# Optimization experiments

Measured on AMD Instinct MI355X. Metric: run time of the kernel, lower is better.

Reference implementation:

```python
import jax, jax.numpy as jnp
import numpy as np

B, S, H, V, E = 64, 20, 128, 50257, 300


def gru(p, x, h):
    # tf.contrib.rnn.GRUCell: r,u = sigmoid([x,h]@Wg + bg); c = tanh([x, r*h]@Wc + bc); h' = u*h + (1-u)*c
    gk, gb, ck, cb = p
    xh = jnp.concatenate([x, h], axis=-1)
    r, u = jnp.split(jax.nn.sigmoid(xh @ gk + gb), 2, axis=-1)
    c = jnp.tanh(jnp.concatenate([x, r * h], axis=-1) @ ck + cb)
    return u * h + (1.0 - u) * c


def setup_inputs() -> dict:
    key = jax.random.key(0)
    ks = jax.random.split(key, 32)
    s = 0.08
    rn = lambda k, shp: (jax.random.normal(k, shp, jnp.float32) * s)
    inp = {}
    inp['x'] = jax.random.randint(ks[0], (B, S), 0, V, dtype=jnp.int32)
    inp['x_length'] = jax.random.randint(ks[1], (B,), 1, S + 1, dtype=jnp.int32)
    inp['y'] = jax.random.randint(ks[2], (B, S), 0, V, dtype=jnp.int32)
    inp['y_length'] = jax.random.randint(ks[3], (B,), 1, S + 1, dtype=jnp.int32)
    inp['embedding'] = jax.random.normal(ks[4], (V, E), jnp.float32) * 0.1
    # encoder GRU: layer0 in=E, layer1 in=H
    inp['e0_gk'] = rn(ks[5], (E + H, 2 * H)); inp['e0_gb'] = rn(ks[6], (2 * H,))
    inp['e0_ck'] = rn(ks[7], (E + H, H));     inp['e0_cb'] = rn(ks[8], (H,))
    inp['e1_gk'] = rn(ks[9], (2 * H, 2 * H)); inp['e1_gb'] = rn(ks[10], (2 * H,))
    inp['e1_ck'] = rn(ks[11], (2 * H, H));    inp['e1_cb'] = rn(ks[12], (H,))
    # decoder GRU: layer0 in = E + attention_size(H) = E+H, layer1 in=H
    inp['d0_gk'] = rn(ks[13], (E + 2 * H, 2 * H)); inp['d0_gb'] = rn(ks[14], (2 * H,))
    inp['d0_ck'] = rn(ks[15], (E + 2 * H, H));     inp['d0_cb'] = rn(ks[16], (H,))
    inp['d1_gk'] = rn(ks[17], (2 * H, 2 * H));     inp['d1_gb'] = rn(ks[18], (2 * H,))
    inp['d1_ck'] = rn(ks[19], (2 * H, H));         inp['d1_cb'] = rn(ks[20], (H,))
    # Bahdanau attention (num_units=H) + attention output layer + vocab projection
    inp['W_mem'] = rn(ks[21], (H, H))
    inp['W_q'] = rn(ks[22], (H, H))
    inp['v_att'] = rn(ks[23], (H,))
    inp['W_attn'] = rn(ks[24], (2 * H, H))
    inp['W_proj'] = rn(ks[25], (H, V))
    inp['b_proj'] = jnp.zeros((V,), jnp.float32)
    return inp


def _forward(x, x_length, y, y_length, embedding,
             e0_gk, e0_gb, e0_ck, e0_cb, e1_gk, e1_gb, e1_ck, e1_cb,
             d0_gk, d0_gb, d0_ck, d0_cb, d1_gk, d1_gb, d1_ck, d1_cb,
             W_mem, W_q, v_att, W_attn, W_proj, b_proj):
    e0 = (e0_gk, e0_gb, e0_ck, e0_cb)
    e1 = (e1_gk, e1_gb, e1_ck, e1_cb)
    d0 = (d0_gk, d0_gb, d0_ck, d0_cb)
    d1 = (d1_gk, d1_gb, d1_ck, d1_cb)
    t_idx = jnp.arange(S)
    x_valid = t_idx[None, :] < x_length[:, None]   # [B,S]
    y_valid = t_idx[None, :] < y_length[:, None]   # [B,S]

    # ---- encoder: 2-layer GRU dynamic_rnn with sequence_length semantics ----
    ex = embedding[x]                               # [B,S,E]
    zeros = jnp.zeros((x.shape[0], H), embedding.dtype)

    def enc_step(carry, inp_t):
        h0, h1 = carry
        xt, vt = inp_t                              # xt [B,E], vt [B,1]
        n0 = gru(e0, xt, h0)
        n1 = gru(e1, n0, h1)
        n0 = jnp.where(vt, n0, h0)                  # copy-through past seq end
        n1 = jnp.where(vt, n1, h1)
        return (n0, n1), jnp.where(vt, n1, 0.0)     # outputs zeroed past seq end

    (h0f, h1f), mem = jax.lax.scan(
        enc_step, (zeros, zeros),
        (ex.transpose(1, 0, 2), x_valid.T[:, :, None]))
    memory = mem.transpose(1, 0, 2)                 # [B,S,H] encoder outputs

    # ---- Bahdanau attention precompute ----
    keys = jnp.einsum('bsh,hu->bsu', memory, W_mem)  # memory_layer(memory)
    neg_inf = jnp.finfo(memory.dtype).min

    # ---- attention decoder (TrainingHelper) ----
    ey = embedding[y]                               # [B,S,E]
    attn0 = jnp.zeros((x.shape[0], H), embedding.dtype)

    def dec_step(carry, inp_t):
        h0, h1, attn = carry
        yt, vt = inp_t                              # yt [B,E], vt [B,1]
        ci = jnp.concatenate([yt, attn], axis=-1)   # cell input = [emb, prev attention]
        n0 = gru(d0, ci, h0)
        n1 = gru(d1, n0, h1)
        q = n1 @ W_q                                # query_layer(cell_output)
        sc = jnp.einsum('bsu,u->bs', jnp.tanh(keys + q[:, None, :]), v_att)
        sc = jnp.where(x_valid, sc, neg_inf)        # memory_sequence_length mask
        al = jax.nn.softmax(sc, axis=-1)            # [B,S]
        ctx = jnp.einsum('bs,bsh->bh', al, memory)  # context
        na = jnp.concatenate([n1, ctx], axis=-1) @ W_attn  # attention_layer (no bias)
        logits = na @ W_proj + b_proj               # projection_layer
        logits = jnp.where(vt, logits, 0.0)         # dynamic_decode zeroes finished emits
        return (n0, n1, na), logits

    _, logits = jax.lax.scan(
        dec_step, (h0f, h1f, attn0),
        (ey.transpose(1, 0, 2), y_valid.T[:, :, None]))
    return logits.transpose(1, 0, 2)                # [B,S,V] rnn_output


def reference(x, x_length, y, y_length, embedding,
              e0_gk, e0_gb, e0_ck, e0_cb, e1_gk, e1_gb, e1_ck, e1_cb,
              d0_gk, d0_gb, d0_ck, d0_cb, d1_gk, d1_gb, d1_ck, d1_cb,
              W_mem, W_q, v_att, W_attn, W_proj, b_proj):
    return _forward(x, x_length, y, y_length, embedding,
                    e0_gk, e0_gb, e0_ck, e0_cb, e1_gk, e1_gb, e1_ck, e1_cb,
                    d0_gk, d0_gb, d0_ck, d0_cb, d1_gk, d1_gb, d1_ck, d1_cb,
                    W_mem, W_q, v_att, W_attn, W_proj, b_proj)
```

## Files before the change

### kernel.cpp

```cpp
#include <hip/hip_runtime.h>
#include <hip/hip_bf16.h>

#define Bb 64
#define Ss 20
#define Hh 128
#define Vv 50257
#define Ee 300
#define Vpad 50304

typedef short bf16x8 __attribute__((ext_vector_type(8)));
typedef float f32x4 __attribute__((ext_vector_type(4)));

__device__ __forceinline__ unsigned short f2bf(float f){
  unsigned u = __float_as_uint(f);
  u += 0x7fff + ((u >> 16) & 1);
  return (unsigned short)(u >> 16);
}
__device__ __forceinline__ float sigm(float x){ return 1.f / (1.f + __expf(-x)); }
__device__ __forceinline__ float tanh_fast(float x){
  float e = __expf(2.f * x);
  return 1.f - 2.f / (e + 1.f);
}

template<int K4>
__device__ __forceinline__ float dotT(const float* __restrict__ w, const float* v){
  float a0 = 0.f, a1 = 0.f, a2 = 0.f, a3 = 0.f;
  const float4* w4 = (const float4*)w;
  const float4* v4 = (const float4*)v;
#pragma unroll
  for (int i = 0; i < K4; i++){
    float4 wv = w4[i]; float4 xv = v4[i];
    a0 = fmaf(wv.x, xv.x, a0); a1 = fmaf(wv.y, xv.y, a1);
    a2 = fmaf(wv.z, xv.z, a2); a3 = fmaf(wv.w, xv.w, a3);
  }
  return (a0 + a1) + (a2 + a3);
}


struct TMat { const float* src; float* dst; int r0, R, C; };
struct TList { TMat m[15]; };

__global__ __launch_bounds__(256) void wtrans_kernel(TList L){
  TMat t = L.m[blockIdx.y];
  int idx = blockIdx.x * 256 + threadIdx.x;
  int total = t.R * t.C;
  if (idx >= total) return;
  int o = idx / t.R;
  int i = idx - o * t.R;
  t.dst[idx] = t.src[(size_t)(t.r0 + i) * t.C + o];
}

__global__ __launch_bounds__(256) void wpt_kernel(const float* __restrict__ Wp,
                                                  unsigned short* __restrict__ Wpt){
  __shared__ unsigned short tile[64][136];
  int n0 = blockIdx.x * 64;
  int tid = threadIdx.x;
  for (int idx = tid; idx < 8192; idx += 256){
    int k = idx >> 6, nn = idx & 63;
    int n = n0 + nn;
    float f = (n < Vv) ? Wp[(size_t)k * Vv + n] : 0.f;
    tile[nn][k] = f2bf(f);
  }
  __syncthreads();
  for (int idx = tid; idx < 1024; idx += 256){
    int nn = idx >> 4, c = idx & 15;
    uint4 v = *reinterpret_cast<const uint4*>(&tile[nn][c * 8]);
    *reinterpret_cast<uint4*>(Wpt + (((size_t)(n0 + nn)) << 7) + c * 8) = v;
  }
}


__global__ __launch_bounds__(256) void pre_kernel(
    const int* __restrict__ x, const int* __restrict__ y, const float* __restrict__ emb,
    const float* __restrict__ egx, const float* __restrict__ ecx,
    const float* __restrict__ egb, const float* __restrict__ ecb,
    const float* __restrict__ dgx, const float* __restrict__ dcx,
    const float* __restrict__ dgb, const float* __restrict__ dcb,
    float* __restrict__ epg, float* __restrict__ epc,
    float* __restrict__ dpg, float* __restrict__ dpc)
{
  __shared__ __align__(16) float er[Ee];
  int tid = threadIdx.x, ti = blockIdx.x, which = blockIdx.y;
  int tok = which ? y[ti] : x[ti];
  if (tid < 75)
    ((float4*)er)[tid] = ((const float4*)(emb + (size_t)tok * Ee))[tid];
  __syncthreads();
  const float* gx = which ? dgx : egx;
  const float* cx = which ? dcx : ecx;
  float accg = (which ? dgb : egb)[tid] + dotT<75>(gx + (size_t)tid * Ee, er);
  (which ? dpg : epg)[ti * 256 + tid] = accg;
  if (tid < 128){
    float accc = (which ? dcb : ecb)[tid] + dotT<75>(cx + (size_t)tid * Ee, er);
    (which ? dpc : epc)[ti * 128 + tid] = accc;
  }
}


__global__ __launch_bounds__(256, 1) void recur2(
    const int* __restrict__ xlen,
    const float* __restrict__ epg, const float* __restrict__ epc,
    const float* __restrict__ dpg, const float* __restrict__ dpc,
    const float* __restrict__ e0_gh_t, const float* __restrict__ e0_ch_t,
    const float* __restrict__ e1_g_t, const float* __restrict__ e1_c_t,
    const float* __restrict__ e1_gb,  const float* __restrict__ e1_cb,
    const float* __restrict__ d0_gah_t, const float* __restrict__ d0_cah_t,
    const float* __restrict__ d1_g_t, const float* __restrict__ d1_c_t,
    const float* __restrict__ d1_gb,  const float* __restrict__ d1_cb,
    const float* __restrict__ W_mem_t, const float* __restrict__ W_q_t,
    const float* __restrict__ W_attn_t, const float* __restrict__ v_att,
    unsigned short* __restrict__ na_bf)
{
  __shared__ __align__(16) float mem_s[Ss][Hh];
  __shared__ __align__(16) float keys_s[Ss][132];
  __shared__ __align__(16) float h0[Hh], h1[Hh], attn[Hh], n0[Hh], n1[Hh], rh[Hh], q[Hh], ctx[Hh];
  __shared__ __align__(16) float gates[2*Hh];
  __shared__ __align__(16) float vatt_s[Hh];
  __shared__ float part[Ss][8], als[Ss];

  const int tid = threadIdx.x, b = blockIdx.x;
  if (tid < Hh){ h0[tid] = 0.f; h1[tid] = 0.f; attn[tid] = 0.f; vatt_s[tid] = v_att[tid]; }
  __syncthreads();
  const int xl = xlen[b];

  for (int t = 0; t < Ss; t++){
    const int tix = b * Ss + t;
    float g = epg[(tix << 8) + tid] + dotT<32>(e0_gh_t + tid * 128, h0);
    gates[tid] = sigm(g);
    __syncthreads();
    if (tid < Hh) rh[tid] = gates[tid] * h0[tid];
    __syncthreads();
    {
      int o = tid >> 1, half = tid & 1;
      float a = dotT<16>(e0_ch_t + o * 128 + half * 64, rh + half * 64);
      a += __shfl_xor(a, 1);
      if (!half){
        float c = tanh_fast(epc[(tix << 7) + o] + a);
        float u = gates[128 + o];
        n0[o] = u * h0[o] + (1.f - u) * c;
      }
    }
    __syncthreads();
    float g1 = e1_gb[tid] + dotT<32>(e1_g_t + tid * 256, n0)
                          + dotT<32>(e1_g_t + tid * 256 + 128, h1);
    gates[tid] = sigm(g1);
    __syncthreads();
    if (tid < Hh) rh[tid] = gates[tid] * h1[tid];
    __syncthreads();
    {
      int o = tid >> 1, half = tid & 1;
      const float* base = e1_c_t + o * 256 + half * 128;
      float a = half ? dotT<32>(base, rh) : dotT<32>(base, n0);
      a += __shfl_xor(a, 1);
      if (!half){
        float c = tanh_fast(e1_cb[o] + a);
        float u = gates[128 + o];
        float nh = u * h1[o] + (1.f - u) * c;
        bool v = (t < xl);
        mem_s[t][o] = v ? nh : 0.f;
        h1[o] = v ? nh : h1[o];
        h0[o] = v ? n0[o] : h0[o];
      }
    }
    __syncthreads();
  }

  for (int idx = tid; idx < Ss * Hh; idx += 256){
    int s = idx >> 7, j = idx & 127;
    keys_s[s][j] = dotT<32>(W_mem_t + j * 128, mem_s[s]);
  }
  __syncthreads();

  for (int t = 0; t < Ss; t++){
    const int tix = b * Ss + t;
    float g = dpg[(tix << 8) + tid] + dotT<32>(d0_gah_t + tid * 256, attn)
                                    + dotT<32>(d0_gah_t + tid * 256 + 128, h0);
    gates[tid] = sigm(g);
    __syncthreads();
    if (tid < Hh) rh[tid] = gates[tid] * h0[tid];
    __syncthreads();
    {
      int o = tid >> 1, half = tid & 1;
      const float* base = d0_cah_t + o * 256 + half * 128;
      float a = half ? dotT<32>(base, rh) : dotT<32>(base, attn);
      a += __shfl_xor(a, 1);
      if (!half){
        float c = tanh_fast(dpc[(tix << 7) + o] + a);
        float u = gates[128 + o];
        float nv = u * h0[o] + (1.f - u) * c;
        n0[o] = nv; h0[o] = nv;
      }
    }
    __syncthreads();
    float g1 = d1_gb[tid] + dotT<32>(d1_g_t + tid * 256, n0)
                          + dotT<32>(d1_g_t + tid * 256 + 128, h1);
    gates[tid] = sigm(g1);
    __syncthreads();
    if (tid < Hh) rh[tid] = gates[tid] * h1[tid];
    __syncthreads();
    {
      int o = tid >> 1, half = tid & 1;
      const float* base = d1_c_t + o * 256 + half * 128;
      float a = half ? dotT<32>(base, rh) : dotT<32>(base, n0);
      a += __shfl_xor(a, 1);
      if (!half){
        float c = tanh_fast(d1_cb[o] + a);
        float u = gates[128 + o];
        float nh = u * h1[o] + (1.f - u) * c;
        n1[o] = nh; h1[o] = nh;
      }
    }
    __syncthreads();
    {
      int o = tid >> 1, half = tid & 1;
      float a = dotT<16>(W_q_t + o * 128 + half * 64, n1 + half * 64);
      a += __shfl_xor(a, 1);
      if (!half) q[o] = a;
    }
    __syncthreads();
    if (tid < Ss * 8){
      int s = tid >> 3, p = tid & 7;
      float a = 0.f;
#pragma unroll
      for (int c2 = 0; c2 < 16; c2++){
        int u2 = p * 16 + c2;
        a += tanh_fast(keys_s[s][u2] + q[u2]) * vatt_s[u2];
      }
      part[s][p] = a;
    }
    __syncthreads();
    if (tid < 64){
      int s = tid;
      bool valid = (s < Ss) && (s < xl);
      float sc = -3.4e38f;
      if (valid){ sc = 0.f;
#pragma unroll
        for (int p = 0; p < 8; p++) sc += part[s][p];
      }
      float mx = sc;
#pragma unroll
      for (int off = 32; off >= 1; off >>= 1) mx = fmaxf(mx, __shfl_xor(mx, off));
      float e = valid ? __expf(sc - mx) : 0.f;
      float sm = e;
#pragma unroll
      for (int off = 32; off >= 1; off >>= 1) sm += __shfl_xor(sm, off);
      if (s < Ss) als[s] = e / sm;
    }
    __syncthreads();
    if (tid < Hh){
      float a = 0.f;
#pragma unroll
      for (int s = 0; s < Ss; s++) a += als[s] * mem_s[s][tid];
      ctx[tid] = a;
    }
    __syncthreads();
    {
      int o = tid >> 1, half = tid & 1;
      const float* base = W_attn_t + o * 256 + half * 128;
      float a = half ? dotT<32>(base, ctx) : dotT<32>(base, n1);
      a += __shfl_xor(a, 1);
      if (!half){
        attn[o] = a;
        na_bf[(tix << 7) + o] = f2bf(a);
      }
    }
    __syncthreads();
  }
}


__global__ __launch_bounds__(256) void proj2(
    const unsigned short* __restrict__ na_bf, const unsigned short* __restrict__ Wpt,
    const float* __restrict__ b_proj, const int* __restrict__ ylen,
    float* __restrict__ out)
{
  __shared__ int yl_s[Bb];
  const int tid = threadIdx.x;
  if (tid < Bb) yl_s[tid] = ylen[tid];
  const int n0 = blockIdx.x * 128, m0 = blockIdx.y * 64;
  const int lane = tid & 63, w = tid >> 6, lm = lane & 15, qq = lane >> 4;

  f32x4 acc[4][2];
#pragma unroll
  for (int mt = 0; mt < 4; mt++){ acc[mt][0] = (f32x4){0,0,0,0}; acc[mt][1] = (f32x4){0,0,0,0}; }

#pragma unroll
  for (int ks = 0; ks < 4; ks++){
    int ko = ks * 32 + qq * 8;
    bf16x8 b0 = *(const bf16x8*)(Wpt + (((size_t)(n0 + w*32 + lm)) << 7) + ko);
    bf16x8 b1 = *(const bf16x8*)(Wpt + (((size_t)(n0 + w*32 + 16 + lm)) << 7) + ko);
#pragma unroll
    for (int mt = 0; mt < 4; mt++){
      bf16x8 a = *(const bf16x8*)(na_bf + (((size_t)(m0 + mt*16 + lm)) << 7) + ko);
      acc[mt][0] = __builtin_amdgcn_mfma_f32_16x16x32_bf16(a, b0, acc[mt][0], 0, 0, 0);
      acc[mt][1] = __builtin_amdgcn_mfma_f32_16x16x32_bf16(a, b1, acc[mt][1], 0, 0, 0);
    }
  }
  __syncthreads();

#pragma unroll
  for (int mt = 0; mt < 4; mt++){
    int row = m0 + mt*16 + qq*4;
#pragma unroll
    for (int n2 = 0; n2 < 2; n2++){
      int col = n0 + w*32 + n2*16 + lm;
      if (col < Vv){
        float bp = b_proj[col];
#pragma unroll
        for (int r = 0; r < 4; r++){
          int rr = row + r;
          int bb = rr / Ss;
          int tt = rr - bb * Ss;
          float val = (tt < yl_s[bb]) ? (acc[mt][n2][r] + bp) : 0.f;
          out[(size_t)rr * Vv + col] = val;
        }
      }
    }
  }
}

extern "C" void kernel_launch(void* const* d_in, const int* in_sizes, int n_in,
                              void* d_out, int out_size, void* d_ws, size_t ws_size,
                              hipStream_t stream) {
  const int*   x        = (const int*)d_in[0];
  const int*   x_length = (const int*)d_in[1];
  const int*   y        = (const int*)d_in[2];
  const int*   y_length = (const int*)d_in[3];
  const float* emb      = (const float*)d_in[4];
  const float* e0_gk = (const float*)d_in[5];  const float* e0_gb = (const float*)d_in[6];
  const float* e0_ck = (const float*)d_in[7];  const float* e0_cb = (const float*)d_in[8];
  const float* e1_gk = (const float*)d_in[9];  const float* e1_gb = (const float*)d_in[10];
  const float* e1_ck = (const float*)d_in[11]; const float* e1_cb = (const float*)d_in[12];
  const float* d0_gk = (const float*)d_in[13]; const float* d0_gb = (const float*)d_in[14];
  const float* d0_ck = (const float*)d_in[15]; const float* d0_cb = (const float*)d_in[16];
  const float* d1_gk = (const float*)d_in[17]; const float* d1_gb = (const float*)d_in[18];
  const float* d1_ck = (const float*)d_in[19]; const float* d1_cb = (const float*)d_in[20];
  const float* W_mem = (const float*)d_in[21]; const float* W_q   = (const float*)d_in[22];
  const float* v_att = (const float*)d_in[23]; const float* W_attn= (const float*)d_in[24];
  const float* W_proj= (const float*)d_in[25]; const float* b_proj= (const float*)d_in[26];
  float* out = (float*)d_out;

  size_t off = 0;
  auto alloc = [&](size_t bytes) -> void* {
    void* p = (char*)d_ws + off;
    off += (bytes + 255) & ~(size_t)255;
    return p;
  };
  unsigned short* Wpt   = (unsigned short*)alloc((size_t)Vpad * 128 * 2);
  unsigned short* na_bf = (unsigned short*)alloc((size_t)Bb * Ss * Hh * 2);
  float* epg = (float*)alloc((size_t)Bb*Ss*256*4);
  float* epc = (float*)alloc((size_t)Bb*Ss*128*4);
  float* dpg = (float*)alloc((size_t)Bb*Ss*256*4);
  float* dpc = (float*)alloc((size_t)Bb*Ss*128*4);
  float* e0_gx_t  = (float*)alloc(256*300*4);
  float* e0_gh_t  = (float*)alloc(256*128*4);
  float* e0_cx_t  = (float*)alloc(128*300*4);
  float* e0_ch_t  = (float*)alloc(128*128*4);
  float* e1_g_t   = (float*)alloc(256*256*4);
  float* e1_c_t   = (float*)alloc(128*256*4);
  float* d0_gx_t  = (float*)alloc(256*300*4);
  float* d0_gah_t = (float*)alloc(256*256*4);
  float* d0_cx_t  = (float*)alloc(128*300*4);
  float* d0_cah_t = (float*)alloc(128*256*4);
  float* d1_g_t   = (float*)alloc(256*256*4);
  float* d1_c_t   = (float*)alloc(128*256*4);
  float* W_mem_t  = (float*)alloc(128*128*4);
  float* W_q_t    = (float*)alloc(128*128*4);
  float* W_attn_t = (float*)alloc(128*256*4);

  TList L;
  L.m[0]  = { e0_gk, e0_gx_t,    0, 300, 256 };
  L.m[1]  = { e0_gk, e0_gh_t,  300, 128, 256 };
  L.m[2]  = { e0_ck, e0_cx_t,    0, 300, 128 };
  L.m[3]  = { e0_ck, e0_ch_t,  300, 128, 128 };
  L.m[4]  = { e1_gk, e1_g_t,     0, 256, 256 };
  L.m[5]  = { e1_ck, e1_c_t,     0, 256, 128 };
  L.m[6]  = { d0_gk, d0_gx_t,    0, 300, 256 };
  L.m[7]  = { d0_gk, d0_gah_t, 300, 256, 256 };
  L.m[8]  = { d0_ck, d0_cx_t,    0, 300, 128 };
  L.m[9]  = { d0_ck, d0_cah_t, 300, 256, 128 };
  L.m[10] = { d1_gk, d1_g_t,     0, 256, 256 };
  L.m[11] = { d1_ck, d1_c_t,     0, 256, 128 };
  L.m[12] = { W_mem, W_mem_t,    0, 128, 128 };
  L.m[13] = { W_q,   W_q_t,      0, 128, 128 };
  L.m[14] = { W_attn,W_attn_t,   0, 256, 128 };

  wtrans_kernel<<<dim3(300, 15), 256, 0, stream>>>(L);
  wpt_kernel<<<Vpad / 64, 256, 0, stream>>>(W_proj, Wpt);
  pre_kernel<<<dim3(Bb * Ss, 2), 256, 0, stream>>>(
      x, y, emb, e0_gx_t, e0_cx_t, e0_gb, e0_cb,
      d0_gx_t, d0_cx_t, d0_gb, d0_cb, epg, epc, dpg, dpc);
  recur2<<<Bb, 256, 0, stream>>>(
      x_length, epg, epc, dpg, dpc,
      e0_gh_t, e0_ch_t, e1_g_t, e1_c_t, e1_gb, e1_cb,
      d0_gah_t, d0_cah_t, d1_g_t, d1_c_t, d1_gb, d1_cb,
      W_mem_t, W_q_t, W_attn_t, v_att, na_bf);
  proj2<<<dim3(Vpad / 128, (Bb * Ss) / 64), 256, 0, stream>>>(
      na_bf, Wpt, b_proj, y_length, out);
}
```

Measured before the change: 1.515 ms.

## Pack recurrent weights as interleaved bf16, restructure GRU steps, retile projection GEMM

```diff
diff --git a/kernel.cpp b/kernel.cpp
--- a/kernel.cpp
+++ b/kernel.cpp
@@ -16,45 +16,59 @@
   u += 0x7fff + ((u >> 16) & 1);
   return (unsigned short)(u >> 16);
 }
+__device__ __forceinline__ float blo(unsigned u){ return __uint_as_float(u << 16); }
+__device__ __forceinline__ float bhi(unsigned u){ return __uint_as_float(u & 0xffff0000u); }
 __device__ __forceinline__ float sigm(float x){ return 1.f / (1.f + __expf(-x)); }
 __device__ __forceinline__ float tanh_fast(float x){
   float e = __expf(2.f * x);
   return 1.f - 2.f / (e + 1.f);
 }
 
-template<int K4>
-__device__ __forceinline__ float dotT(const float* __restrict__ w, const float* v){
-  float a0 = 0.f, a1 = 0.f, a2 = 0.f, a3 = 0.f;
-  const float4* w4 = (const float4*)w;
-  const float4* v4 = (const float4*)v;
-#pragma unroll
-  for (int i = 0; i < K4; i++){
-    float4 wv = w4[i]; float4 xv = v4[i];
-    a0 = fmaf(wv.x, xv.x, a0); a1 = fmaf(wv.y, xv.y, a1);
-    a2 = fmaf(wv.z, xv.z, a2); a3 = fmaf(wv.w, xv.w, a3);
+template<int K8, int O>
+__device__ __forceinline__ float dotP(const uint4* __restrict__ wp, int o, const float* x){
+  float a0=0.f, a1=0.f, a2=0.f, a3=0.f;
+  const float4* x4 = (const float4*)x;
+#pragma unroll
+  for (int kk = 0; kk < K8; kk++){
+    uint4 u = wp[kk*O + o];
+    float4 xa = x4[2*kk], xb = x4[2*kk+1];
+    a0 = fmaf(blo(u.x), xa.x, a0); a1 = fmaf(bhi(u.x), xa.y, a1);
+    a2 = fmaf(blo(u.y), xa.z, a2); a3 = fmaf(bhi(u.y), xa.w, a3);
+    a0 = fmaf(blo(u.z), xb.x, a0); a1 = fmaf(bhi(u.z), xb.y, a1);
+    a2 = fmaf(blo(u.w), xb.z, a2); a3 = fmaf(bhi(u.w), xb.w, a3);
   }
   return (a0 + a1) + (a2 + a3);
 }
 
 
-struct TMat { const float* src; float* dst; int r0, R, C; };
-struct TList { TMat m[15]; };
-
-__global__ __launch_bounds__(256) void wtrans_kernel(TList L){
-  TMat t = L.m[blockIdx.y];
+struct PD { const float* src; uint4* dst; int r0, K, O; };
+struct PL { PD m[15]; };
+
+__global__ __launch_bounds__(256) void pack_kernel(PL L){
+  PD p = L.m[blockIdx.y];
+  int K8 = (p.K + 7) >> 3;
   int idx = blockIdx.x * 256 + threadIdx.x;
-  int total = t.R * t.C;
-  if (idx >= total) return;
-  int o = idx / t.R;
-  int i = idx - o * t.R;
-  t.dst[idx] = t.src[(size_t)(t.r0 + i) * t.C + o];
-}
-
-__global__ __launch_bounds__(256) void wpt_kernel(const float* __restrict__ Wp,
-                                                  unsigned short* __restrict__ Wpt){
+  if (idx >= K8 * p.O) return;
+  int kk = idx / p.O, o = idx - kk * p.O;
+  unsigned w[8];
+#pragma unroll
+  for (int j = 0; j < 8; j++){
+    int k = 8*kk + j;
+    float f = (k < p.K) ? p.src[(size_t)(p.r0 + k) * p.O + o] : 0.f;
+    w[j] = f2bf(f);
+  }
+  uint4 u;
+  u.x = w[0] | (w[1] << 16);
+  u.y = w[2] | (w[3] << 16);
+  u.z = w[4] | (w[5] << 16);
+  u.w = w[6] | (w[7] << 16);
+  p.dst[idx] = u;
+}
+
+__global__ __launch_bounds__(256) void wpt2_kernel(const float* __restrict__ Wp,
+                                                   unsigned short* __restrict__ W2){
   __shared__ unsigned short tile[64][136];
-  int n0 = blockIdx.x * 64;
-  int tid = threadIdx.x;
+  int n0 = blockIdx.x * 64, tid = threadIdx.x;
   for (int idx = tid; idx < 8192; idx += 256){
     int k = idx >> 6, nn = idx & 63;
     int n = n0 + nn;
@@ -63,159 +77,140 @@
   }
   __syncthreads();
   for (int idx = tid; idx < 1024; idx += 256){
-    int nn = idx >> 4, c = idx & 15;
+    int c = idx >> 6, nn = idx & 63;
     uint4 v = *reinterpret_cast<const uint4*>(&tile[nn][c * 8]);
-    *reinterpret_cast<uint4*>(Wpt + (((size_t)(n0 + nn)) << 7) + c * 8) = v;
-  }
-}
-
-
-__global__ __launch_bounds__(256) void pre_kernel(
+    int n = n0 + nn;
+    size_t dst = (((size_t)(n >> 4) * 16 + c) * 16 + (n & 15)) * 8;
+    *reinterpret_cast<uint4*>(W2 + dst) = v;
+  }
+}
+
+
+__global__ __launch_bounds__(256) void pre2(
     const int* __restrict__ x, const int* __restrict__ y, const float* __restrict__ emb,
-    const float* __restrict__ egx, const float* __restrict__ ecx,
+    const uint4* __restrict__ egx, const uint4* __restrict__ ecx,
     const float* __restrict__ egb, const float* __restrict__ ecb,
-    const float* __restrict__ dgx, const float* __restrict__ dcx,
+    const uint4* __restrict__ dgx, const uint4* __restrict__ dcx,
     const float* __restrict__ dgb, const float* __restrict__ dcb,
     float* __restrict__ epg, float* __restrict__ epc,
     float* __restrict__ dpg, float* __restrict__ dpc)
 {
-  __shared__ __align__(16) float er[Ee];
+  __shared__ __align__(16) float er[304];
   int tid = threadIdx.x, ti = blockIdx.x, which = blockIdx.y;
   int tok = which ? y[ti] : x[ti];
   if (tid < 75)
     ((float4*)er)[tid] = ((const float4*)(emb + (size_t)tok * Ee))[tid];
+  if (tid < 4) er[300 + tid] = 0.f;
   __syncthreads();
-  const float* gx = which ? dgx : egx;
-  const float* cx = which ? dcx : ecx;
-  float accg = (which ? dgb : egb)[tid] + dotT<75>(gx + (size_t)tid * Ee, er);
-  (which ? dpg : epg)[ti * 256 + tid] = accg;
+  const uint4* gx = which ? dgx : egx;
+  const uint4* cx = which ? dcx : ecx;
+  float g = (which ? dgb : egb)[tid] + dotP<38,256>(gx, tid, er);
+  (which ? dpg : epg)[ti * 256 + tid] = g;
   if (tid < 128){
-    float accc = (which ? dcb : ecb)[tid] + dotT<75>(cx + (size_t)tid * Ee, er);
-    (which ? dpc : epc)[ti * 128 + tid] = accc;
-  }
-}
-
-
-__global__ __launch_bounds__(256, 1) void recur2(
+    float c = (which ? dcb : ecb)[tid] + dotP<38,128>(cx, tid, er);
+    (which ? dpc : epc)[ti * 128 + tid] = c;
+  }
+}
+
+
+__global__ __launch_bounds__(256, 1) void recur3(
     const int* __restrict__ xlen,
     const float* __restrict__ epg, const float* __restrict__ epc,
     const float* __restrict__ dpg, const float* __restrict__ dpc,
-    const float* __restrict__ e0_gh_t, const float* __restrict__ e0_ch_t,
-    const float* __restrict__ e1_g_t, const float* __restrict__ e1_c_t,
-    const float* __restrict__ e1_gb,  const float* __restrict__ e1_cb,
-    const float* __restrict__ d0_gah_t, const float* __restrict__ d0_cah_t,
-    const float* __restrict__ d1_g_t, const float* __restrict__ d1_c_t,
-    const float* __restrict__ d1_gb,  const float* __restrict__ d1_cb,
-    const float* __restrict__ W_mem_t, const float* __restrict__ W_q_t,
-    const float* __restrict__ W_attn_t, const float* __restrict__ v_att,
-    unsigned short* __restrict__ na_bf)
+    const uint4* __restrict__ e0g, const uint4* __restrict__ e0c,
+    const uint4* __restrict__ e1g, const uint4* __restrict__ e1c,
+    const float* __restrict__ e1_gb, const float* __restrict__ e1_cb,
+    const uint4* __restrict__ d0g, const uint4* __restrict__ d0c,
+    const uint4* __restrict__ d1g, const uint4* __restrict__ d1c,
+    const float* __restrict__ d1_gb, const float* __restrict__ d1_cb,
+    const uint4* __restrict__ wm, const uint4* __restrict__ wq,
+    const uint4* __restrict__ wat, const float* __restrict__ v_att,
+    unsigned short* __restrict__ na2)
 {
   __shared__ __align__(16) float mem_s[Ss][Hh];
   __shared__ __align__(16) float keys_s[Ss][132];
-  __shared__ __align__(16) float h0[Hh], h1[Hh], attn[Hh], n0[Hh], n1[Hh], rh[Hh], q[Hh], ctx[Hh];
-  __shared__ __align__(16) float gates[2*Hh];
+  __shared__ __align__(16) float h0[Hh];
+  __shared__ __align__(16) float cat0[256], cat0c[256], cat1[256], cat1c[256], catA[256];
+  __shared__ __align__(16) float gates[256];
+  __shared__ __align__(16) float qv[Hh];
   __shared__ __align__(16) float vatt_s[Hh];
   __shared__ float part[Ss][8], als[Ss];
 
   const int tid = threadIdx.x, b = blockIdx.x;
-  if (tid < Hh){ h0[tid] = 0.f; h1[tid] = 0.f; attn[tid] = 0.f; vatt_s[tid] = v_att[tid]; }
+  if (tid < 128){ h0[tid] = 0.f; cat1[128 + tid] = 0.f; vatt_s[tid] = v_att[tid]; }
   __syncthreads();
   const int xl = xlen[b];
 
   for (int t = 0; t < Ss; t++){
     const int tix = b * Ss + t;
-    float g = epg[(tix << 8) + tid] + dotT<32>(e0_gh_t + tid * 128, h0);
-    gates[tid] = sigm(g);
-    __syncthreads();
-    if (tid < Hh) rh[tid] = gates[tid] * h0[tid];
-    __syncthreads();
     {
-      int o = tid >> 1, half = tid & 1;
-      float a = dotT<16>(e0_ch_t + o * 128 + half * 64, rh + half * 64);
-      a += __shfl_xor(a, 1);
-      if (!half){
-        float c = tanh_fast(epc[(tix << 7) + o] + a);
-        float u = gates[128 + o];
-        n0[o] = u * h0[o] + (1.f - u) * c;
-      }
-    }
-    __syncthreads();
-    float g1 = e1_gb[tid] + dotT<32>(e1_g_t + tid * 256, n0)
-                          + dotT<32>(e1_g_t + tid * 256 + 128, h1);
-    gates[tid] = sigm(g1);
-    __syncthreads();
-    if (tid < Hh) rh[tid] = gates[tid] * h1[tid];
+      float gs = sigm(epg[tix * 256 + tid] + dotP<16,256>(e0g, tid, h0));
+      gates[tid] = gs;
+      if (tid < 128) cat0c[tid] = gs * h0[tid];
+    }
+    __syncthreads();
+    if (tid < 128){
+      float c = tanh_fast(epc[tix * 128 + tid] + dotP<16,128>(e0c, tid, cat0c));
+      float u = gates[128 + tid];
+      cat1[tid] = u * h0[tid] + (1.f - u) * c;
+    }
     __syncthreads();
     {
-      int o = tid >> 1, half = tid & 1;
-      const float* base = e1_c_t + o * 256 + half * 128;
-      float a = half ? dotT<32>(base, rh) : dotT<32>(base, n0);
-      a += __shfl_xor(a, 1);
-      if (!half){
-        float c = tanh_fast(e1_cb[o] + a);
-        float u = gates[128 + o];
-        float nh = u * h1[o] + (1.f - u) * c;
-        bool v = (t < xl);
-        mem_s[t][o] = v ? nh : 0.f;
-        h1[o] = v ? nh : h1[o];
-        h0[o] = v ? n0[o] : h0[o];
-      }
+      float gs = sigm(e1_gb[tid] + dotP<32,256>(e1g, tid, cat1));
+      gates[tid] = gs;
+      if (tid < 128){ cat1c[tid] = cat1[tid]; cat1c[128 + tid] = gs * cat1[128 + tid]; }
+    }
+    __syncthreads();
+    if (tid < 128){
+      float c = tanh_fast(e1_cb[tid] + dotP<32,128>(e1c, tid, cat1c));
+      float u = gates[128 + tid];
+      float h1o = cat1[128 + tid];
+      float nh = u * h1o + (1.f - u) * c;
+      bool v = (t < xl);
+      mem_s[t][tid] = v ? nh : 0.f;
+      cat1[128 + tid] = v ? nh : h1o;
+      h0[tid] = v ? cat1[tid] : h0[tid];
     }
     __syncthreads();
   }
 
   for (int idx = tid; idx < Ss * Hh; idx += 256){
     int s = idx >> 7, j = idx & 127;
-    keys_s[s][j] = dotT<32>(W_mem_t + j * 128, mem_s[s]);
-  }
+    keys_s[s][j] = dotP<16,128>(wm, j, mem_s[s]);
+  }
+  if (tid < 128){ cat0[tid] = 0.f; cat0[128 + tid] = h0[tid]; }
   __syncthreads();
 
   for (int t = 0; t < Ss; t++){
     const int tix = b * Ss + t;
-    float g = dpg[(tix << 8) + tid] + dotT<32>(d0_gah_t + tid * 256, attn)
-                                    + dotT<32>(d0_gah_t + tid * 256 + 128, h0);
-    gates[tid] = sigm(g);
-    __syncthreads();
-    if (tid < Hh) rh[tid] = gates[tid] * h0[tid];
-    __syncthreads();
     {
-      int o = tid >> 1, half = tid & 1;
-      const float* base = d0_cah_t + o * 256 + half * 128;
-      float a = half ? dotT<32>(base, rh) : dotT<32>(base, attn);
-      a += __shfl_xor(a, 1);
-      if (!half){
-        float c = tanh_fast(dpc[(tix << 7) + o] + a);
-        float u = gates[128 + o];
-        float nv = u * h0[o] + (1.f - u) * c;
-        n0[o] = nv; h0[o] = nv;
-      }
-    }
-    __syncthreads();
-    float g1 = d1_gb[tid] + dotT<32>(d1_g_t + tid * 256, n0)
-                          + dotT<32>(d1_g_t + tid * 256 + 128, h1);
-    gates[tid] = sigm(g1);
-    __syncthreads();
-    if (tid < Hh) rh[tid] = gates[tid] * h1[tid];
+      float gs = sigm(dpg[tix * 256 + tid] + dotP<32,256>(d0g, tid, cat0));
+      gates[tid] = gs;
+      if (tid < 128){ cat0c[tid] = cat0[tid]; cat0c[128 + tid] = gs * cat0[128 + tid]; }
+    }
+    __syncthreads();
+    if (tid < 128){
+      float c = tanh_fast(dpc[tix * 128 + tid] + dotP<32,128>(d0c, tid, cat0c));
+      float u = gates[128 + tid];
+      float nv = u * cat0[128 + tid] + (1.f - u) * c;
+      cat1[tid] = nv; cat0[128 + tid] = nv;
+    }
     __syncthreads();
     {
-      int o = tid >> 1, half = tid & 1;
-      const float* base = d1_c_t + o * 256 + half * 128;
-      float a = half ? dotT<32>(base, rh) : dotT<32>(base, n0);
-      a += __shfl_xor(a, 1);
-      if (!half){
-        float c = tanh_fast(d1_cb[o] + a);
-        float u = gates[128 + o];
-        float nh = u * h1[o] + (1.f - u) * c;
-        n1[o] = nh; h1[o] = nh;
-      }
-    }
-    __syncthreads();
-    {
-      int o = tid >> 1, half = tid & 1;
-      float a = dotT<16>(W_q_t + o * 128 + half * 64, n1 + half * 64);
-      a += __shfl_xor(a, 1);
-      if (!half) q[o] = a;
-    }
+      float gs = sigm(d1_gb[tid] + dotP<32,256>(d1g, tid, cat1));
+      gates[tid] = gs;
+      if (tid < 128){ cat1c[tid] = cat1[tid]; cat1c[128 + tid] = gs * cat1[128 + tid]; }
+    }
+    __syncthreads();
+    if (tid < 128){
+      float c = tanh_fast(d1_cb[tid] + dotP<32,128>(d1c, tid, cat1c));
+      float u = gates[128 + tid];
+      float h1o = cat1[128 + tid];
+      float nh = u * h1o + (1.f - u) * c;
+      catA[tid] = nh; cat1[128 + tid] = nh;
+    }
+    __syncthreads();
+    if (tid < 128) qv[tid] = dotP<16,128>(wq, tid, catA);
     __syncthreads();
     if (tid < Ss * 8){
       int s = tid >> 3, p = tid & 7;
@@ -223,7 +218,7 @@
 #pragma unroll
       for (int c2 = 0; c2 < 16; c2++){
         int u2 = p * 16 + c2;
-        a += tanh_fast(keys_s[s][u2] + q[u2]) * vatt_s[u2];
+        a += tanh_fast(keys_s[s][u2] + qv[u2]) * vatt_s[u2];
       }
       part[s][p] = a;
     }
@@ -246,73 +241,80 @@
       if (s < Ss) als[s] = e / sm;
     }
     __syncthreads();
-    if (tid < Hh){
+    if (tid < 128){
       float a = 0.f;
 #pragma unroll
       for (int s = 0; s < Ss; s++) a += als[s] * mem_s[s][tid];
-      ctx[tid] = a;
-    }
-    __syncthreads();
-    {
-      int o = tid >> 1, half = tid & 1;
-      const float* base = W_attn_t + o * 256 + half * 128;
-      float a = half ? dotT<32>(base, ctx) : dotT<32>(base, n1);
-      a += __shfl_xor(a, 1);
-      if (!half){
-        attn[o] = a;
-        na_bf[(tix << 7) + o] = f2bf(a);
-      }
-    }
-    __syncthreads();
-  }
-}
-
-
-__global__ __launch_bounds__(256) void proj2(
-    const unsigned short* __restrict__ na_bf, const unsigned short* __restrict__ Wpt,
+      catA[128 + tid] = a;
+    }
+    __syncthreads();
+    if (tid < 128){
+      float a = dotP<32,128>(wat, tid, catA);
+      cat0[tid] = a;
+      na2[(((size_t)(tix >> 4) * 16 + (tid >> 3)) * 16 + (tix & 15)) * 8 + (tid & 7)] = f2bf(a);
+    }
+    __syncthreads();
+  }
+}
+
+
+__global__ __launch_bounds__(256) void proj3(
+    const unsigned short* __restrict__ A2, const unsigned short* __restrict__ W2,
     const float* __restrict__ b_proj, const int* __restrict__ ylen,
     float* __restrict__ out)
 {
   __shared__ int yl_s[Bb];
   const int tid = threadIdx.x;
   if (tid < Bb) yl_s[tid] = ylen[tid];
-  const int n0 = blockIdx.x * 128, m0 = blockIdx.y * 64;
-  const int lane = tid & 63, w = tid >> 6, lm = lane & 15, qq = lane >> 4;
-
-  f32x4 acc[4][2];
-#pragma unroll
-  for (int mt = 0; mt < 4; mt++){ acc[mt][0] = (f32x4){0,0,0,0}; acc[mt][1] = (f32x4){0,0,0,0}; }
+  __syncthreads();
+  const int n0 = blockIdx.x * 128, m0 = blockIdx.y * 128;
+  const int w = tid >> 6, lane = tid & 63, lm = lane & 15, qq = lane >> 4;
+  const int wr = w >> 1, wc = w & 1;
+  const int mtb = (m0 >> 4) + wr * 4, ntb = (n0 >> 4) + wc * 4;
+
+  f32x4 acc[4][4];
+#pragma unroll
+  for (int mt = 0; mt < 4; mt++)
+#pragma unroll
+    for (int nt = 0; nt < 4; nt++) acc[mt][nt] = (f32x4){0.f,0.f,0.f,0.f};
 
 #pragma unroll
   for (int ks = 0; ks < 4; ks++){
-    int ko = ks * 32 + qq * 8;
-    bf16x8 b0 = *(const bf16x8*)(Wpt + (((size_t)(n0 + w*32 + lm)) << 7) + ko);
-    bf16x8 b1 = *(const bf16x8*)(Wpt + (((size_t)(n0 + w*32 + 16 + lm)) << 7) + ko);
-#pragma unroll
-    for (int mt = 0; mt < 4; mt++){
-      bf16x8 a = *(const bf16x8*)(na_bf + (((size_t)(m0 + mt*16 + lm)) << 7) + ko);
-      acc[mt][0] = __builtin_amdgcn_mfma_f32_16x16x32_bf16(a, b0, acc[mt][0], 0, 0, 0);
-      acc[mt][1] = __builtin_amdgcn_mfma_f32_16x16x32_bf16(a, b1, acc[mt][1], 0, 0, 0);
-    }
-  }
-  __syncthreads();
+    int kc = ks * 4 + qq;
+    bf16x8 bfr[4], afr[4];
+#pragma unroll
+    for (int nt = 0; nt < 4; nt++)
+      bfr[nt] = *(const bf16x8*)(W2 + (((size_t)(ntb + nt) * 16 + kc) * 16 + lm) * 8);
+#pragma unroll
+    for (int mt = 0; mt < 4; mt++)
+      afr[mt] = *(const bf16x8*)(A2 + (((size_t)(mtb + mt) * 16 + kc) * 16 + lm) * 8);
+#pragma unroll
+    for (int mt = 0; mt < 4; mt++)
+#pragma unroll
+      for (int nt = 0; nt < 4; nt++)
+        acc[mt][nt] = __builtin_amdgcn_mfma_f32_16x16x32_bf16(afr[mt], bfr[nt], acc[mt][nt], 0, 0, 0);
+  }
+
+  float bp[4];
+#pragma unroll
+  for (int nt = 0; nt < 4; nt++){
+    int col = n0 + wc * 64 + nt * 16 + lm;
+    bp[nt] = (col < Vv) ? b_proj[col] : 0.f;
+  }
 
 #pragma unroll
   for (int mt = 0; mt < 4; mt++){
-    int row = m0 + mt*16 + qq*4;
-#pragma unroll
-    for (int n2 = 0; n2 < 2; n2++){
-      int col = n0 + w*32 + n2*16 + lm;
-      if (col < Vv){
-        float bp = b_proj[col];
-#pragma unroll
-        for (int r = 0; r < 4; r++){
-          int rr = row + r;
-          int bb = rr / Ss;
-          int tt = rr - bb * Ss;
-          float val = (tt < yl_s[bb]) ? (acc[mt][n2][r] + bp) : 0.f;
-          out[(size_t)rr * Vv + col] = val;
-        }
+    int rowb = m0 + wr * 64 + mt * 16 + qq * 4;
+#pragma unroll
+    for (int r = 0; r < 4; r++){
+      int rr = rowb + r;
+      int bb = rr / Ss, tt = rr - bb * Ss;
+      bool vr = tt < yl_s[bb];
+#pragma unroll
+      for (int nt = 0; nt < 4; nt++){
+        int col = n0 + wc * 64 + nt * 16 + lm;
+        if (col < Vv)
+          out[(size_t)rr * Vv + col] = vr ? (acc[mt][nt][r] + bp[nt]) : 0.f;
       }
     }
   }
@@ -345,55 +347,55 @@
     off += (bytes + 255) & ~(size_t)255;
     return p;
   };
-  unsigned short* Wpt   = (unsigned short*)alloc((size_t)Vpad * 128 * 2);
-  unsigned short* na_bf = (unsigned short*)alloc((size_t)Bb * Ss * Hh * 2);
+  unsigned short* W2  = (unsigned short*)alloc((size_t)Vpad * 128 * 2);
+  unsigned short* na2 = (unsigned short*)alloc((size_t)Bb * Ss * Hh * 2);
   float* epg = (float*)alloc((size_t)Bb*Ss*256*4);
   float* epc = (float*)alloc((size_t)Bb*Ss*128*4);
   float* dpg = (float*)alloc((size_t)Bb*Ss*256*4);
   float* dpc = (float*)alloc((size_t)Bb*Ss*128*4);
-  float* e0_gx_t  = (float*)alloc(256*300*4);
-  float* e0_gh_t  = (float*)alloc(256*128*4);
-  float* e0_cx_t  = (float*)alloc(128*300*4);
-  float* e0_ch_t  = (float*)alloc(128*128*4);
-  float* e1_g_t   = (float*)alloc(256*256*4);
-  float* e1_c_t   = (float*)alloc(128*256*4);
-  float* d0_gx_t  = (float*)alloc(256*300*4);
-  float* d0_gah_t = (float*)alloc(256*256*4);
-  float* d0_cx_t  = (float*)alloc(128*300*4);
-  float* d0_cah_t = (float*)alloc(128*256*4);
-  float* d1_g_t   = (float*)alloc(256*256*4);
-  float* d1_c_t   = (float*)alloc(128*256*4);
-  float* W_mem_t  = (float*)alloc(128*128*4);
-  float* W_q_t    = (float*)alloc(128*128*4);
-  float* W_attn_t = (float*)alloc(128*256*4);
-
-  TList L;
-  L.m[0]  = { e0_gk, e0_gx_t,    0, 300, 256 };
-  L.m[1]  = { e0_gk, e0_gh_t,  300, 128, 256 };
-  L.m[2]  = { e0_ck, e0_cx_t,    0, 300, 128 };
-  L.m[3]  = { e0_ck, e0_ch_t,  300, 128, 128 };
-  L.m[4]  = { e1_gk, e1_g_t,     0, 256, 256 };
-  L.m[5]  = { e1_ck, e1_c_t,     0, 256, 128 };
-  L.m[6]  = { d0_gk, d0_gx_t,    0, 300, 256 };
-  L.m[7]  = { d0_gk, d0_gah_t, 300, 256, 256 };
-  L.m[8]  = { d0_ck, d0_cx_t,    0, 300, 128 };
-  L.m[9]  = { d0_ck, d0_cah_t, 300, 256, 128 };
-  L.m[10] = { d1_gk, d1_g_t,     0, 256, 256 };
-  L.m[11] = { d1_ck, d1_c_t,     0, 256, 128 };
-  L.m[12] = { W_mem, W_mem_t,    0, 128, 128 };
-  L.m[13] = { W_q,   W_q_t,      0, 128, 128 };
-  L.m[14] = { W_attn,W_attn_t,   0, 256, 128 };
-
-  wtrans_kernel<<<dim3(300, 15), 256, 0, stream>>>(L);
-  wpt_kernel<<<Vpad / 64, 256, 0, stream>>>(W_proj, Wpt);
-  pre_kernel<<<dim3(Bb * Ss, 2), 256, 0, stream>>>(
-      x, y, emb, e0_gx_t, e0_cx_t, e0_gb, e0_cb,
-      d0_gx_t, d0_cx_t, d0_gb, d0_cb, epg, epc, dpg, dpc);
-  recur2<<<Bb, 256, 0, stream>>>(
+  uint4* e0g  = (uint4*)alloc(16*256*16);
+  uint4* e0c  = (uint4*)alloc(16*128*16);
+  uint4* e1g  = (uint4*)alloc(32*256*16);
+  uint4* e1c  = (uint4*)alloc(32*128*16);
+  uint4* d0g  = (uint4*)alloc(32*256*16);
+  uint4* d0c  = (uint4*)alloc(32*128*16);
+  uint4* d1g  = (uint4*)alloc(32*256*16);
+  uint4* d1c  = (uint4*)alloc(32*128*16);
+  uint4* wm   = (uint4*)alloc(16*128*16);
+  uint4* wq   = (uint4*)alloc(16*128*16);
+  uint4* wat  = (uint4*)alloc(32*128*16);
+  uint4* e0gx = (uint4*)alloc(38*256*16);
+  uint4* e0cx = (uint4*)alloc(38*128*16);
+  uint4* d0gx = (uint4*)alloc(38*256*16);
+  uint4* d0cx = (uint4*)alloc(38*128*16);
+
+  PL L;
+  L.m[0]  = { e0_gk, e0g,  300, 128, 256 };
+  L.m[1]  = { e0_ck, e0c,  300, 128, 128 };
+  L.m[2]  = { e1_gk, e1g,    0, 256, 256 };
+  L.m[3]  = { e1_ck, e1c,    0, 256, 128 };
+  L.m[4]  = { d0_gk, d0g,  300, 256, 256 };
+  L.m[5]  = { d0_ck, d0c,  300, 256, 128 };
+  L.m[6]  = { d1_gk, d1g,    0, 256, 256 };
+  L.m[7]  = { d1_ck, d1c,    0, 256, 128 };
+  L.m[8]  = { W_mem, wm,     0, 128, 128 };
+  L.m[9]  = { W_q,   wq,     0, 128, 128 };
+  L.m[10] = { W_attn,wat,    0, 256, 128 };
+  L.m[11] = { e0_gk, e0gx,   0, 300, 256 };
+  L.m[12] = { e0_ck, e0cx,   0, 300, 128 };
+  L.m[13] = { d0_gk, d0gx,   0, 300, 256 };
+  L.m[14] = { d0_ck, d0cx,   0, 300, 128 };
+
+  pack_kernel<<<dim3(38, 15), 256, 0, stream>>>(L);
+  wpt2_kernel<<<Vpad / 64, 256, 0, stream>>>(W_proj, W2);
+  pre2<<<dim3(Bb * Ss, 2), 256, 0, stream>>>(
+      x, y, emb, e0gx, e0cx, e0_gb, e0_cb,
+      d0gx, d0cx, d0_gb, d0_cb, epg, epc, dpg, dpc);
+  recur3<<<Bb, 256, 0, stream>>>(
       x_length, epg, epc, dpg, dpc,
-      e0_gh_t, e0_ch_t, e1_g_t, e1_c_t, e1_gb, e1_cb,
-      d0_gah_t, d0_cah_t, d1_g_t, d1_c_t, d1_gb, d1_cb,
-      W_mem_t, W_q_t, W_attn_t, v_att, na_bf);
-  proj2<<<dim3(Vpad / 128, (Bb * Ss) / 64), 256, 0, stream>>>(
-      na_bf, Wpt, b_proj, y_length, out);
-}
+      e0g, e0c, e1g, e1c, e1_gb, e1_cb,
+      d0g, d0c, d1g, d1c, d1_gb, d1_cb,
+      wm, wq, wat, v_att, na2);
+  proj3<<<dim3(Vpad / 128, (Bb * Ss) / 128), 256, 0, stream>>>(
+      na2, W2, b_proj, y_length, out);
+}
```

Result: slower. 1.684 ms (+11.1%).
